# Kernel tuning notes

Measured on AMD Instinct MI355X. Metric: run time of the kernel, lower is better.

Reference implementation:

```python
import jax, jax.numpy as jnp
import numpy as np

B, T, DIM = 8, 4096, 1024
HEADS = 16
WS = [10, 20]
SHIFTS = [5, 10]
DIM_IN = DIM // 2        # bottleneck_ratio=0.5
DIM_BR = DIM_IN // 2     # per-branch channels
H_BR = HEADS // 2        # per-branch heads
EPS = 1e-6


def setup_inputs() -> dict:
    key = jax.random.key(0)
    ks = jax.random.split(key, 12)
    w = lambda k, s: (jax.random.normal(k, s) * 0.02).astype(jnp.float32)
    z = lambda n: jnp.zeros((n,), jnp.float32)
    return {
        "x": jax.random.normal(ks[0], (B, T, DIM), jnp.float32),
        "down_w": w(ks[1], (DIM, DIM_IN)), "down_b": z(DIM_IN),
        "up_w": w(ks[2], (DIM_IN, DIM)), "up_b": z(DIM),
        "norm1_w": jnp.ones((DIM_IN,), jnp.float32),
        "norm2_w": jnp.ones((DIM,), jnp.float32),
        "qkv1_w": w(ks[3], (DIM_BR, 3 * DIM_BR)), "qkv1_b": z(3 * DIM_BR),
        "proj1_w": w(ks[4], (DIM_BR, DIM_BR)), "proj1_b": z(DIM_BR),
        "rpb1": w(ks[5], (2 * WS[0] - 1, H_BR)),
        "qkv2_w": w(ks[6], (DIM_BR, 3 * DIM_BR)), "qkv2_b": z(3 * DIM_BR),
        "proj2_w": w(ks[7], (DIM_BR, DIM_BR)), "proj2_b": z(DIM_BR),
        "rpb2": w(ks[8], (2 * WS[1] - 1, H_BR)),
        "ffn_w1": w(ks[9], (DIM, 2 * DIM)), "ffn_b1": z(2 * DIM),
        "ffn_w2": w(ks[10], (2 * DIM, DIM)), "ffn_b2": z(DIM),
    }


def rmsnorm(x, w):
    return x * jax.lax.rsqrt(jnp.mean(x * x, axis=-1, keepdims=True) + EPS) * w


def _branch(x, window, shift, qkv_w, qkv_b, pw, pb, rpb, heads):
    # x: [B, T, C]; shifted-window attention along T with relative position bias
    Bx, Tn, C = x.shape
    pad = (-Tn) % window
    xp = jnp.pad(x, ((0, 0), (0, pad), (0, 0)))
    Tp = Tn + pad
    nW = Tp // window
    hd = C // heads
    scale = hd ** -0.5

    if shift > 0:
        xp = jnp.roll(xp, -shift, axis=1)
        m = np.zeros(Tp, np.float32)
        m[Tp - window:Tp - shift] = 1.0
        m[Tp - shift:] = 2.0
        mw = m.reshape(nW, window)
        amask = jnp.asarray(np.where(mw[:, :, None] != mw[:, None, :], -100.0, 0.0).astype(np.float32))  # [nW,w,w]
    else:
        amask = None

    xw = xp.reshape(Bx, nW, window, C)
    qkv = (xw @ qkv_w + qkv_b).reshape(Bx, nW, window, 3, heads, hd)
    q, k, v = qkv[:, :, :, 0], qkv[:, :, :, 1], qkv[:, :, :, 2]  # [B,nW,w,h,hd]

    attn = jnp.einsum('bnqhd,bnkhd->bnhqk', q * scale, k)  # [B,nW,h,w,w]

    coords = np.arange(window)
    ridx = coords[:, None] - coords[None, :] + window - 1      # [w,w]
    bias = jnp.transpose(rpb[ridx], (2, 0, 1))                 # [h,w,w]
    attn = attn + bias[None, None]
    if amask is not None:
        attn = attn + amask[None, :, None]

    attn = jax.nn.softmax(attn, axis=-1)
    out = jnp.einsum('bnhqk,bnkhd->bnqhd', attn, v).reshape(Bx, nW, window, C)
    out = out @ pw + pb
    out = out.reshape(Bx, Tp, C)
    if shift > 0:
        out = jnp.roll(out, shift, axis=1)
    return out[:, :Tn]


def reference(x, down_w, down_b, up_w, up_b, norm1_w, norm2_w,
              qkv1_w, qkv1_b, proj1_w, proj1_b, rpb1,
              qkv2_w, qkv2_b, proj2_w, proj2_b, rpb2,
              ffn_w1, ffn_b1, ffn_w2, ffn_b2):
    residual = x
    xi = rmsnorm(x @ down_w + down_b, norm1_w)           # [B,T,DIM_IN]
    x1, x2 = xi[..., :DIM_BR], xi[..., DIM_BR:]
    o1 = _branch(x1, WS[0], SHIFTS[0], qkv1_w, qkv1_b, proj1_w, proj1_b, rpb1, H_BR)
    o2 = _branch(x2, WS[1], SHIFTS[1], qkv2_w, qkv2_b, proj2_w, proj2_b, rpb2, H_BR)
    xc = jnp.concatenate([o1, o2], axis=-1) @ up_w + up_b
    x = residual + xc
    h = rmsnorm(x, norm2_w)
    ffn = jax.nn.gelu(h @ ffn_w1 + ffn_b1, approximate=False) @ ffn_w2 + ffn_b2
    return x + ffn
```

## Files before the change

kernel.cpp:

```cpp
#include <hip/hip_runtime.h>
#include <hip/hip_bf16.h>
#include <math.h>

typedef __bf16 bf16x8_t __attribute__((ext_vector_type(8)));
typedef float f32x4_t __attribute__((ext_vector_type(4)));
typedef __hip_bfloat16 bf16;

__device__ __forceinline__ void gload_lds16(const bf16* gsrc, unsigned short* ldst) {
  __builtin_amdgcn_global_load_lds(
      (const __attribute__((address_space(1))) unsigned int*)gsrc,
      (__attribute__((address_space(3))) unsigned int*)ldst, 16, 0, 0);
}

__global__ __launch_bounds__(256) void f2b_kernel(const float* __restrict__ in,
                                                  bf16* __restrict__ out, size_t n) {
  size_t i = ((size_t)blockIdx.x * 256 + threadIdx.x) * 4;
  if (i + 4 <= n) {
    float4 v = *reinterpret_cast<const float4*>(in + i);
    union { bf16 b[4]; ushort4 u; } cv;
    cv.b[0] = __float2bfloat16(v.x);
    cv.b[1] = __float2bfloat16(v.y);
    cv.b[2] = __float2bfloat16(v.z);
    cv.b[3] = __float2bfloat16(v.w);
    *reinterpret_cast<ushort4*>(out + i) = cv.u;
  } else {
    for (; i < n; ++i) out[i] = __float2bfloat16(in[i]);
  }
}

__global__ __launch_bounds__(256) void transpose_f2b_kernel(const float* __restrict__ in,
                                                            bf16* __restrict__ out,
                                                            int K, int N) {
  __shared__ float t[32][33];
  int n0 = blockIdx.x * 32, k0 = blockIdx.y * 32;
  int tx = threadIdx.x & 31, ty = threadIdx.x >> 5;
#pragma unroll
  for (int i = 0; i < 32; i += 8)
    t[ty + i][tx] = in[(size_t)(k0 + ty + i) * N + n0 + tx];
  __syncthreads();
#pragma unroll
  for (int i = 0; i < 32; i += 8)
    out[(size_t)(n0 + ty + i) * K + k0 + tx] = __float2bfloat16(t[tx][ty + i]);
}

__global__ __launch_bounds__(256) void rmsnorm_kernel(const float* __restrict__ in,
                                                      const float* __restrict__ w,
                                                      bf16* __restrict__ out, int C) {
  int row = blockIdx.x;
  const float* r = in + (size_t)row * C;
  int tid = threadIdx.x;
  float ss = 0.f;
  for (int c = tid; c < C; c += 256) { float v = r[c]; ss += v * v; }
#pragma unroll
  for (int o = 32; o > 0; o >>= 1) ss += __shfl_down(ss, o, 64);
  __shared__ float part[4];
  if ((tid & 63) == 0) part[tid >> 6] = ss;
  __syncthreads();
  float inv = rsqrtf((part[0] + part[1] + part[2] + part[3]) / (float)C + 1e-6f);
  bf16* orow = out + (size_t)row * C;
  for (int c = tid; c < C; c += 256) orow[c] = __float2bfloat16(r[c] * inv * w[c]);
}

__global__ __launch_bounds__(256) void gather_kernel(const bf16* __restrict__ xi,
                                                     bf16* __restrict__ xb,
                                                     int Tp, int Tn, int shift, int coff) {
  size_t i = (size_t)blockIdx.x * 256 + threadIdx.x;
  int c = (int)(i & 255);
  size_t bt = i >> 8;
  int t = (int)(bt % (size_t)Tp);
  int b = (int)(bt / (size_t)Tp);
  int src = t + shift; if (src >= Tp) src -= Tp;
  bf16 v = __float2bfloat16(0.f);
  if (src < Tn) v = xi[(((size_t)b * Tn + src) << 9) + coff + c];
  xb[i] = v;
}

template <int W, int SHIFT>
__global__ void attn_kernel(const bf16* __restrict__ qkv, const float* __restrict__ rpb,
                            bf16* __restrict__ out, int nW, int Tp) {
  int blk = blockIdx.x;
  int b = blk / nW, n = blk % nW;
  int pair = threadIdx.x;
  if (pair >= 8 * W) return;
  int h = pair / W, qi = pair % W;
  size_t base = ((size_t)b * Tp + (size_t)n * W) * 768;
  float qv[32];
#pragma unroll
  for (int d = 0; d < 32; ++d) qv[d] = __bfloat162float(qkv[base + (size_t)qi * 768 + h * 32 + d]);
  const float scale = 0.17677669529663689f;
  float sc[W];
  float mx = -1e30f;
  for (int k = 0; k < W; ++k) {
    const bf16* kr = qkv + base + (size_t)k * 768 + 256 + h * 32;
    float dot = 0.f;
#pragma unroll
    for (int d = 0; d < 32; ++d) dot += qv[d] * __bfloat162float(kr[d]);
    float s = dot * scale + rpb[(qi - k + W - 1) * 8 + h];
    if (n == nW - 1) {
      bool lq = qi < (W - SHIFT), lk = k < (W - SHIFT);
      if (lq != lk) s -= 100.0f;
    }
    sc[k] = s;
    mx = fmaxf(mx, s);
  }
  float l = 0.f;
  for (int k = 0; k < W; ++k) { sc[k] = expf(sc[k] - mx); l += sc[k]; }
  float inv = 1.0f / l;
  float ov[32];
#pragma unroll
  for (int d = 0; d < 32; ++d) ov[d] = 0.f;
  for (int k = 0; k < W; ++k) {
    const bf16* vr = qkv + base + (size_t)k * 768 + 512 + h * 32;
    float p = sc[k];
#pragma unroll
    for (int d = 0; d < 32; ++d) ov[d] += p * __bfloat162float(vr[d]);
  }
  bf16* orow = out + ((size_t)b * Tp + (size_t)n * W + qi) * 256 + h * 32;
#pragma unroll
  for (int d = 0; d < 32; ++d) orow[d] = __float2bfloat16(ov[d] * inv);
}

template <int MODE>
__global__ __launch_bounds__(256) void gemm_kernel(
    const bf16* __restrict__ A, const bf16* __restrict__ Wt,
    const float* __restrict__ bias,
    float* outF, bf16* outB, const float* resid,
    int M, int N, int K, int ldc, int Tp, int Tn, int shift, int coff) {
  __shared__ unsigned short lA[3][128 * 32];
  __shared__ unsigned short lB[3][128 * 32];
  int tid = threadIdx.x;
  int wave = tid >> 6, lane = tid & 63;

  int nx = gridDim.x;
  int nwg = nx * gridDim.y;
  int id = blockIdx.y * nx + blockIdx.x;
  int q = nwg >> 3, r = nwg & 7;
  int xcd = id & 7, pos = id >> 3;
  int swz = (xcd < r ? xcd * (q + 1) : r * (q + 1) + (xcd - r) * q) + pos;
  int bx = swz % nx, by = swz / nx;

  int m0 = by * 128, n0 = bx * 128;
  int wm = (wave >> 1) * 64, wn = (wave & 1) * 64;
  int ml = lane & 15, cc = lane >> 4;
  f32x4_t acc[4][4] = {};

  int lrow = lane >> 2;
  int pchunk = lane & 3;

  auto stage = [&](int buf, int k0) {
#pragma unroll
    for (int j = 0; j < 2; ++j) {
      int rr = wave * 32 + j * 16;
      int row = rr + lrow;
      int scol = (pchunk ^ ((row >> 1) & 3)) * 8;
      int gr = m0 + row; if (gr > M - 1) gr = M - 1;
      gload_lds16(A + (size_t)gr * K + k0 + scol, &lA[buf][rr * 32]);
      int nr = n0 + row;
      gload_lds16(Wt + (size_t)nr * K + k0 + scol, &lB[buf][rr * 32]);
    }
  };
  auto compute = [&](int buf) {
    const unsigned short* sA = lA[buf];
    const unsigned short* sB = lB[buf];
    bf16x8_t fa[4], fb[4];
#pragma unroll
    for (int t = 0; t < 4; ++t) {
      int ra = wm + t * 16 + ml;
      fa[t] = *reinterpret_cast<const bf16x8_t*>(&sA[ra * 32 + ((cc ^ ((ra >> 1) & 3)) << 3)]);
      int rb = wn + t * 16 + ml;
      fb[t] = *reinterpret_cast<const bf16x8_t*>(&sB[rb * 32 + ((cc ^ ((rb >> 1) & 3)) << 3)]);
    }
    __builtin_amdgcn_s_setprio(1);
#pragma unroll
    for (int mt = 0; mt < 4; ++mt)
#pragma unroll
      for (int nt = 0; nt < 4; ++nt)
        acc[mt][nt] = __builtin_amdgcn_mfma_f32_16x16x32_bf16(fa[mt], fb[nt], acc[mt][nt], 0, 0, 0);
    __builtin_amdgcn_s_setprio(0);
  };

  int NT = K >> 5;
  stage(0, 0);
  stage(1, 32);
  stage(2, 64);
  int cur = 0;
  for (int t = 0; t < NT; ++t) {
    int rem = NT - 1 - t;
    if (rem >= 2)      asm volatile("s_waitcnt vmcnt(8)" ::: "memory");
    else if (rem == 1) asm volatile("s_waitcnt vmcnt(4)" ::: "memory");
    else               asm volatile("s_waitcnt vmcnt(0)" ::: "memory");
    __builtin_amdgcn_s_barrier();
    compute(cur);
    __builtin_amdgcn_s_barrier();
    if (t + 3 < NT) stage(cur, (t + 3) * 32);
    cur = cur + 1; if (cur == 3) cur = 0;
  }

  int rbase = (lane >> 4) * 4;
#pragma unroll
  for (int mt = 0; mt < 4; ++mt)
#pragma unroll
    for (int nt = 0; nt < 4; ++nt)
#pragma unroll
      for (int i = 0; i < 4; ++i) {
        int row = m0 + wm + mt * 16 + rbase + i;
        int col = n0 + wn + nt * 16 + ml;
        if (row >= M) continue;
        float v = acc[mt][nt][i] + bias[col];
        if (MODE == 0) {
          outF[(size_t)row * ldc + col] = v;
        } else if (MODE == 1) {
          outB[(size_t)row * ldc + col] = __float2bfloat16(v);
        } else if (MODE == 2) {
          outF[(size_t)row * ldc + col] = v + resid[(size_t)row * ldc + col];
        } else if (MODE == 3) {
          v = 0.5f * v * (1.0f + erff(v * 0.70710678118654752f));
          outB[(size_t)row * ldc + col] = __float2bfloat16(v);
        } else if (MODE == 5) {
          int b = row / Tp;
          int t = row - b * Tp;
          int i2 = t + shift; if (i2 >= Tp) i2 -= Tp;
          if (i2 < Tn)
            outB[((size_t)b * Tn + i2) * ldc + coff + col] = __float2bfloat16(v);
        }
      }
}

extern "C" void kernel_launch(void* const* d_in, const int* in_sizes, int n_in,
                              void* d_out, int out_size, void* d_ws, size_t ws_size,
                              hipStream_t stream) {
  const float* x       = (const float*)d_in[0];
  const float* down_w  = (const float*)d_in[1];
  const float* down_b  = (const float*)d_in[2];
  const float* up_w    = (const float*)d_in[3];
  const float* up_b    = (const float*)d_in[4];
  const float* norm1_w = (const float*)d_in[5];
  const float* norm2_w = (const float*)d_in[6];
  const float* qkv1_w  = (const float*)d_in[7];
  const float* qkv1_b  = (const float*)d_in[8];
  const float* proj1_w = (const float*)d_in[9];
  const float* proj1_b = (const float*)d_in[10];
  const float* rpb1    = (const float*)d_in[11];
  const float* qkv2_w  = (const float*)d_in[12];
  const float* qkv2_b  = (const float*)d_in[13];
  const float* proj2_w = (const float*)d_in[14];
  const float* proj2_b = (const float*)d_in[15];
  const float* rpb2    = (const float*)d_in[16];
  const float* ffn_w1  = (const float*)d_in[17];
  const float* ffn_b1  = (const float*)d_in[18];
  const float* ffn_w2  = (const float*)d_in[19];
  const float* ffn_b2  = (const float*)d_in[20];
  float* out = (float*)d_out;

  const int Bb = 8, T = 4096, DIM = 1024, DIM_IN = 512;
  const int Tp = 4100, Tn = T;
  const int M  = Bb * T;
  const int Mp = Bb * Tp;
  const int nW1 = Tp / 10, nW2 = Tp / 20;

  char* ws = (char*)d_ws;
  const size_t MB = 1ull << 20;
  size_t wo = 0;
  auto walloc = [&](size_t elems) {
    bf16* p = (bf16*)(ws + wo);
    wo += ((elems * 2 + 255) & ~(size_t)255);
    return p;
  };
  bf16* w_down  = walloc(1024 * 512);
  bf16* w_up    = walloc(512 * 1024);
  bf16* w_qkv1  = walloc(256 * 768);
  bf16* w_proj1 = walloc(256 * 256);
  bf16* w_qkv2  = walloc(256 * 768);
  bf16* w_proj2 = walloc(256 * 256);
  bf16* w_ffn1  = walloc(1024 * 2048);
  bf16* w_ffn2  = walloc(2048 * 1024);
  bf16*  xbf     = (bf16*)(ws + 12 * MB);
  bf16*  xb1     = (bf16*)(ws + 12 * MB);
  bf16*  xb2     = (bf16*)(ws + 29 * MB);
  bf16*  att1    = (bf16*)(ws + 46 * MB);
  bf16*  att2    = (bf16*)(ws + 63 * MB);
  float* y1      = (float*)(ws + 80 * MB);
  bf16*  concatb = (bf16*)(ws + 80 * MB);
  bf16*  hbuf    = (bf16*)(ws + 80 * MB);
  bf16*  xi      = (bf16*)(ws + 144 * MB);
  bf16*  qkv1buf = (bf16*)(ws + 176 * MB);
  bf16*  qkv2buf = (bf16*)(ws + 225 * MB);
  bf16*  gbuf    = (bf16*)(ws + 144 * MB);

  auto cvt = [&](const float* src, bf16* dst, size_t n) {
    int grid = (int)((n / 4 + 255) / 256);
    hipLaunchKernelGGL(f2b_kernel, dim3(grid), dim3(256), 0, stream, src, dst, n);
  };
  auto tr = [&](const float* src, bf16* dst, int K, int N) {
    hipLaunchKernelGGL(transpose_f2b_kernel, dim3(N / 32, K / 32), dim3(256), 0, stream,
                       src, dst, K, N);
  };
  cvt(x, xbf, (size_t)M * DIM);
  tr(down_w, w_down, 1024, 512);
  tr(up_w, w_up, 512, 1024);
  tr(qkv1_w, w_qkv1, 256, 768);
  tr(proj1_w, w_proj1, 256, 256);
  tr(qkv2_w, w_qkv2, 256, 768);
  tr(proj2_w, w_proj2, 256, 256);
  tr(ffn_w1, w_ffn1, 1024, 2048);
  tr(ffn_w2, w_ffn2, 2048, 1024);

  auto gemm = [&](auto modeTag, const bf16* A, const bf16* Wt, const float* bias,
                  float* oF, bf16* oB, const float* res,
                  int Mm, int Nn, int Kk, int ldc, int tp, int tn, int sh, int co) {
    constexpr int MODE = decltype(modeTag)::value;
    hipLaunchKernelGGL((gemm_kernel<MODE>), dim3(Nn / 128, (Mm + 127) / 128), dim3(256), 0,
                       stream, A, Wt, bias, oF, oB, res, Mm, Nn, Kk, ldc, tp, tn, sh, co);
  };
  using I0 = std::integral_constant<int, 0>;
  using I1 = std::integral_constant<int, 1>;
  using I2 = std::integral_constant<int, 2>;
  using I3 = std::integral_constant<int, 3>;
  using I5 = std::integral_constant<int, 5>;

  gemm(I0{}, xbf, w_down, down_b, y1, nullptr, nullptr, M, DIM_IN, DIM, DIM_IN, 0, 0, 0, 0);
  hipLaunchKernelGGL(rmsnorm_kernel, dim3(M), dim3(256), 0, stream, y1, norm1_w, xi, DIM_IN);
  hipLaunchKernelGGL(gather_kernel, dim3(Mp), dim3(256), 0, stream, xi, xb1, Tp, Tn, 5, 0);
  hipLaunchKernelGGL(gather_kernel, dim3(Mp), dim3(256), 0, stream, xi, xb2, Tp, Tn, 10, 256);
  gemm(I1{}, xb1, w_qkv1, qkv1_b, nullptr, qkv1buf, nullptr, Mp, 768, 256, 768, 0, 0, 0, 0);
  gemm(I1{}, xb2, w_qkv2, qkv2_b, nullptr, qkv2buf, nullptr, Mp, 768, 256, 768, 0, 0, 0, 0);
  hipLaunchKernelGGL((attn_kernel<10, 5>), dim3(Bb * nW1), dim3(128), 0, stream,
                     qkv1buf, rpb1, att1, nW1, Tp);
  hipLaunchKernelGGL((attn_kernel<20, 10>), dim3(Bb * nW2), dim3(192), 0, stream,
                     qkv2buf, rpb2, att2, nW2, Tp);
  gemm(I5{}, att1, w_proj1, proj1_b, nullptr, concatb, nullptr, Mp, 256, 256, 512, Tp, Tn, 5, 0);
  gemm(I5{}, att2, w_proj2, proj2_b, nullptr, concatb, nullptr, Mp, 256, 256, 512, Tp, Tn, 10, 256);
  gemm(I2{}, concatb, w_up, up_b, out, nullptr, x, M, DIM, DIM_IN, DIM, 0, 0, 0, 0);
  hipLaunchKernelGGL(rmsnorm_kernel, dim3(M), dim3(256), 0, stream, out, norm2_w, hbuf, DIM);
  gemm(I3{}, hbuf, w_ffn1, ffn_b1, nullptr, gbuf, nullptr, M, 2048, DIM, 2048, 0, 0, 0, 0);
  gemm(I2{}, gbuf, w_ffn2, ffn_b2, out, nullptr, out, M, DIM, 2048, DIM, 0, 0, 0, 0);
  (void)in_sizes; (void)n_in; (void)out_size; (void)ws_size;
}
```

Measured before the change: 1.542 ms.

## Add 256x256-tile 8-wave GEMM kernel for large dense projections

Adds a new GEMM kernel with 256x256 output tiles, 512 threads, double-buffered LDS split into two K halves, and async global-to-LDS loads. It interleaves staging with MFMA phases using explicit vmcnt waits and s_setprio, and applies an XCD-aware workgroup swizzle. It is used for the down, up and both FFN projections, while the old 128-tile kernel is kept for the qkv and proj GEMMs. The larger tiles give more data reuse per tile at the cost of fewer workgroups and higher register and LDS pressure, and the kernel assumes M and N are multiples of 256.

```diff
diff --git a/kernel.cpp b/kernel.cpp
--- a/kernel.cpp
+++ b/kernel.cpp
@@ -1,6 +1,7 @@
 #include <hip/hip_runtime.h>
 #include <hip/hip_bf16.h>
 #include <math.h>
+#include <type_traits>
 
 typedef __bf16 bf16x8_t __attribute__((ext_vector_type(8)));
 typedef float f32x4_t __attribute__((ext_vector_type(4)));
@@ -207,23 +208,145 @@
         int col = n0 + wn + nt * 16 + ml;
         if (row >= M) continue;
         float v = acc[mt][nt][i] + bias[col];
+        if (MODE == 1) {
+          outB[(size_t)row * ldc + col] = __float2bfloat16(v);
+        } else if (MODE == 5) {
+          int b = row / Tp;
+          int t2 = row - b * Tp;
+          int i2 = t2 + shift; if (i2 >= Tp) i2 -= Tp;
+          if (i2 < Tn)
+            outB[((size_t)b * Tn + i2) * ldc + coff + col] = __float2bfloat16(v);
+        }
+      }
+  (void)outF; (void)resid;
+}
+
+template <int MODE>
+__global__ __launch_bounds__(512, 2) void gemm256_kernel(
+    const bf16* __restrict__ A, const bf16* __restrict__ Wt,
+    const float* __restrict__ bias,
+    float* outF, bf16* outB, const float* resid,
+    int M, int N, int K, int ldc) {
+  __shared__ unsigned short sA[2][2][256 * 32];
+  __shared__ unsigned short sB[2][2][256 * 32];
+  int tid = threadIdx.x;
+  int wave = tid >> 6, lane = tid & 63;
+
+  int nx = gridDim.x;
+  int nwg = nx * gridDim.y;
+  int id = blockIdx.y * nx + blockIdx.x;
+  int q8 = nwg >> 3, r8 = nwg & 7;
+  int xcd = id & 7, pos = id >> 3;
+  int swzid = (xcd < r8 ? xcd * (q8 + 1) : r8 * (q8 + 1) + (xcd - r8) * q8) + pos;
+  int bx = swzid % nx, by = swzid / nx;
+  int m0 = by * 256, n0 = bx * 256;
+
+  int wr = wave >> 2, wc = wave & 3;
+  int ml = lane & 15;
+  f32x4_t acc[8][4] = {};
+
+  int rowoff0 = (wave * 2 + 0) * 16 + (lane >> 2);
+  int rowoff1 = (wave * 2 + 1) * 16 + (lane >> 2);
+  int gcol = ((lane & 3) ^ ((lane >> 3) & 3)) << 3;
+  const bf16* pA0 = A + (size_t)(m0 + rowoff0) * K + gcol;
+  const bf16* pA1 = A + (size_t)(m0 + rowoff1) * K + gcol;
+  const bf16* pB0 = Wt + (size_t)(n0 + rowoff0) * K + gcol;
+  const bf16* pB1 = Wt + (size_t)(n0 + rowoff1) * K + gcol;
+  unsigned dst = (unsigned)(wave * 2) * 512;
+
+  int pc = ((lane >> 4) ^ ((ml >> 1) & 3)) & 3;
+  int baseA = (wr * 128 + ml) * 32 + pc * 8;
+  int baseB = (wc * 64 + ml) * 32 + pc * 8;
+
+  auto stageA = [&](int kt, int kh) {
+    int ko = kt * 64 + kh * 32;
+    gload_lds16(pA0 + ko, &sA[kt & 1][kh][dst]);
+    gload_lds16(pA1 + ko, &sA[kt & 1][kh][dst + 512]);
+  };
+  auto stageB = [&](int kt, int kh) {
+    int ko = kt * 64 + kh * 32;
+    gload_lds16(pB0 + ko, &sB[kt & 1][kh][dst]);
+    gload_lds16(pB1 + ko, &sB[kt & 1][kh][dst + 512]);
+  };
+
+  bf16x8_t fa[8], fb[4];
+  auto loadfrags = [&](int cur, int kh) {
+    const unsigned short* mA = &sA[cur][kh][0];
+    const unsigned short* mB = &sB[cur][kh][0];
+#pragma unroll
+    for (int rf = 0; rf < 8; ++rf)
+      fa[rf] = *reinterpret_cast<const bf16x8_t*>(&mA[baseA + rf * 512]);
+#pragma unroll
+    for (int cf = 0; cf < 4; ++cf)
+      fb[cf] = *reinterpret_cast<const bf16x8_t*>(&mB[baseB + cf * 512]);
+  };
+  auto mfma8x2 = [&](auto chc) {
+    constexpr int CH = decltype(chc)::value;
+    __builtin_amdgcn_s_setprio(1);
+#pragma unroll
+    for (int cf = 0; cf < 2; ++cf)
+#pragma unroll
+      for (int rf = 0; rf < 8; ++rf)
+        acc[rf][CH * 2 + cf] = __builtin_amdgcn_mfma_f32_16x16x32_bf16(
+            fa[rf], fb[CH * 2 + cf], acc[rf][CH * 2 + cf], 0, 0, 0);
+    __builtin_amdgcn_s_setprio(0);
+  };
+  using C0 = std::integral_constant<int, 0>;
+  using C1 = std::integral_constant<int, 1>;
+
+  int KT = K >> 6;
+  stageA(0, 0); stageB(0, 0); stageA(0, 1); stageB(0, 1);
+  stageA(1, 0); stageB(1, 0); stageA(1, 1);
+
+  for (int g = 0; g < KT; ++g) {
+    int cur = g & 1;
+    if (g + 1 < KT) stageB(g + 1, 1);
+    if (g == KT - 1) { asm volatile("s_waitcnt vmcnt(4)" ::: "memory"); }
+    else             { asm volatile("s_waitcnt vmcnt(10)" ::: "memory"); }
+    __builtin_amdgcn_s_barrier();
+    asm volatile("" ::: "memory");
+    loadfrags(cur, 0);
+    mfma8x2(C0{});
+    __builtin_amdgcn_s_barrier();
+    if (g + 2 < KT) stageA(g + 2, 0);
+    __builtin_amdgcn_s_barrier();
+    mfma8x2(C1{});
+    __builtin_amdgcn_s_barrier();
+    if (g + 2 < KT) stageB(g + 2, 0);
+    if (g < KT - 2)       { asm volatile("s_waitcnt vmcnt(10)" ::: "memory"); }
+    else if (g == KT - 2) { asm volatile("s_waitcnt vmcnt(8)" ::: "memory"); }
+    else                  { asm volatile("s_waitcnt vmcnt(0)" ::: "memory"); }
+    __builtin_amdgcn_s_barrier();
+    asm volatile("" ::: "memory");
+    loadfrags(cur, 1);
+    mfma8x2(C0{});
+    __builtin_amdgcn_s_barrier();
+    if (g + 2 < KT) stageA(g + 2, 1);
+    __builtin_amdgcn_s_barrier();
+    mfma8x2(C1{});
+    __builtin_amdgcn_s_barrier();
+  }
+
+  int rbase = (lane >> 4) * 4;
+#pragma unroll
+  for (int rf = 0; rf < 8; ++rf)
+#pragma unroll
+    for (int cf = 0; cf < 4; ++cf)
+#pragma unroll
+      for (int i = 0; i < 4; ++i) {
+        int row = m0 + wr * 128 + rf * 16 + rbase + i;
+        int col = n0 + wc * 64 + cf * 16 + ml;
+        float v = acc[rf][cf][i] + bias[col];
         if (MODE == 0) {
           outF[(size_t)row * ldc + col] = v;
-        } else if (MODE == 1) {
-          outB[(size_t)row * ldc + col] = __float2bfloat16(v);
         } else if (MODE == 2) {
           outF[(size_t)row * ldc + col] = v + resid[(size_t)row * ldc + col];
         } else if (MODE == 3) {
           v = 0.5f * v * (1.0f + erff(v * 0.70710678118654752f));
           outB[(size_t)row * ldc + col] = __float2bfloat16(v);
-        } else if (MODE == 5) {
-          int b = row / Tp;
-          int t = row - b * Tp;
-          int i2 = t + shift; if (i2 >= Tp) i2 -= Tp;
-          if (i2 < Tn)
-            outB[((size_t)b * Tn + i2) * ldc + coff + col] = __float2bfloat16(v);
         }
       }
+  (void)M; (void)N;
 }
 
 extern "C" void kernel_launch(void* const* d_in, const int* in_sizes, int n_in,
@@ -312,13 +435,19 @@
     hipLaunchKernelGGL((gemm_kernel<MODE>), dim3(Nn / 128, (Mm + 127) / 128), dim3(256), 0,
                        stream, A, Wt, bias, oF, oB, res, Mm, Nn, Kk, ldc, tp, tn, sh, co);
   };
+  auto gemm256 = [&](auto modeTag, const bf16* A, const bf16* Wt, const float* bias,
+                     float* oF, bf16* oB, const float* res, int Mm, int Nn, int Kk, int ldc) {
+    constexpr int MODE = decltype(modeTag)::value;
+    hipLaunchKernelGGL((gemm256_kernel<MODE>), dim3(Nn / 256, Mm / 256), dim3(512), 0,
+                       stream, A, Wt, bias, oF, oB, res, Mm, Nn, Kk, ldc);
+  };
   using I0 = std::integral_constant<int, 0>;
   using I1 = std::integral_constant<int, 1>;
   using I2 = std::integral_constant<int, 2>;
   using I3 = std::integral_constant<int, 3>;
   using I5 = std::integral_constant<int, 5>;
 
-  gemm(I0{}, xbf, w_down, down_b, y1, nullptr, nullptr, M, DIM_IN, DIM, DIM_IN, 0, 0, 0, 0);
+  gemm256(I0{}, xbf, w_down, down_b, y1, nullptr, nullptr, M, DIM_IN, DIM, DIM_IN);
   hipLaunchKernelGGL(rmsnorm_kernel, dim3(M), dim3(256), 0, stream, y1, norm1_w, xi, DIM_IN);
   hipLaunchKernelGGL(gather_kernel, dim3(Mp), dim3(256), 0, stream, xi, xb1, Tp, Tn, 5, 0);
   hipLaunchKernelGGL(gather_kernel, dim3(Mp), dim3(256), 0, stream, xi, xb2, Tp, Tn, 10, 256);
@@ -330,9 +459,9 @@
                      qkv2buf, rpb2, att2, nW2, Tp);
   gemm(I5{}, att1, w_proj1, proj1_b, nullptr, concatb, nullptr, Mp, 256, 256, 512, Tp, Tn, 5, 0);
   gemm(I5{}, att2, w_proj2, proj2_b, nullptr, concatb, nullptr, Mp, 256, 256, 512, Tp, Tn, 10, 256);
-  gemm(I2{}, concatb, w_up, up_b, out, nullptr, x, M, DIM, DIM_IN, DIM, 0, 0, 0, 0);
+  gemm256(I2{}, concatb, w_up, up_b, out, nullptr, x, M, DIM, DIM_IN, DIM);
   hipLaunchKernelGGL(rmsnorm_kernel, dim3(M), dim3(256), 0, stream, out, norm2_w, hbuf, DIM);
-  gemm(I3{}, hbuf, w_ffn1, ffn_b1, nullptr, gbuf, nullptr, M, 2048, DIM, 2048, 0, 0, 0, 0);
-  gemm(I2{}, gbuf, w_ffn2, ffn_b2, out, nullptr, out, M, DIM, 2048, DIM, 0, 0, 0, 0);
+  gemm256(I3{}, hbuf, w_ffn1, ffn_b1, nullptr, gbuf, nullptr, M, 2048, DIM, 2048);
+  gemm256(I2{}, gbuf, w_ffn2, ffn_b2, out, nullptr, out, M, DIM, 2048, DIM);
   (void)in_sizes; (void)n_in; (void)out_size; (void)ws_size;
 }
```

After: 1.408 ms. 8.7% less time.
